# Kernel optimization log

Hardware: AMD Instinct MI355X
Metric: run time of the kernel (lower is better)

Reference implementation:

```python
import jax, jax.numpy as jnp
import numpy as np

B, N, C, L = 32, 1024, 128, 4

def setup_inputs() -> dict:
    key = jax.random.key(0)
    ks = jax.random.split(key, 8)
    x = jax.random.normal(ks[0], (B, N, C), dtype=jnp.float32)
    # binary adjacency: nonzero entries become unit-weight edges (edge weights unused in module)
    adj = jax.random.randint(ks[1], (B, N, N), 0, 2).astype(jnp.float32)
    mask = jnp.ones((B, N), dtype=jnp.float32)
    s = 1.0 / np.sqrt(C)
    weight = jax.random.uniform(ks[2], (L, C, C), minval=-s, maxval=s, dtype=jnp.float32)
    w_ih = jax.random.uniform(ks[3], (L, 3 * C, C), minval=-s, maxval=s, dtype=jnp.float32)
    w_hh = jax.random.uniform(ks[4], (L, 3 * C, C), minval=-s, maxval=s, dtype=jnp.float32)
    b_ih = jax.random.uniform(ks[5], (L, 3 * C), minval=-s, maxval=s, dtype=jnp.float32)
    b_hh = jax.random.uniform(ks[6], (L, 3 * C), minval=-s, maxval=s, dtype=jnp.float32)
    return {"x": x, "adj": adj, "mask": mask, "weight": weight,
            "w_ih": w_ih, "w_hh": w_hh, "b_ih": b_ih, "b_hh": b_hh}

def _gru_cell(m, h, w_ih, w_hh, b_ih, b_hh):
    # PyTorch GRUCell, gate order (r, z, n)
    gx = m @ w_ih.T + b_ih
    gh = h @ w_hh.T + b_hh
    xr, xz, xn = jnp.split(gx, 3, axis=-1)
    hr, hz, hn = jnp.split(gh, 3, axis=-1)
    r = jax.nn.sigmoid(xr + hr)
    z = jax.nn.sigmoid(xz + hz)
    n = jnp.tanh(xn + r * hn)
    return (1.0 - z) * n + z * h

def reference(x, adj, mask, weight, w_ih, w_hh, b_ih, b_hh):
    h = x  # [B, N, C]; in_channels == out_channels so no zero-padding needed
    for i in range(L):
        hw = jnp.einsum('bnc,cd->bnd', h, weight[i])
        # scatter-add of messages source->target == A^T @ (h W), unit edge weights
        m = jnp.einsum('bjn,bjd->bnd', adj, hw)
        h = _gru_cell(m, h, w_ih[i], w_hh[i], b_ih[i], b_hh[i])
    return h * mask[:, :, None]
```

## Files before the change

kernel.cpp:

```cpp
#include <hip/hip_runtime.h>
#include <stdint.h>


#define NB 32
#define NN 1024
#define NC 128
#define NL 4
#define MTOT (NB * NN)

#define KT 64
#define PITCH 72
#define MP 136
#define MSKP 260

typedef __attribute__((ext_vector_type(8))) short s16x8;
typedef __attribute__((ext_vector_type(4))) float f32x4;
typedef __attribute__((ext_vector_type(2))) unsigned int u32x2;
typedef __attribute__((ext_vector_type(4))) unsigned int u32x4;
typedef unsigned short U16;
typedef unsigned int U32;

__device__ __forceinline__ U16 f2bf(float f) {
    union { float f; U32 u; } v; v.f = f;
    return (U16)((v.u + 0x7FFFu + ((v.u >> 16) & 1u)) >> 16);
}
__device__ __forceinline__ float bf2f(U16 h) {
    union { U32 u; float f; } v; v.u = ((U32)h) << 16;
    return v.f;
}
__device__ __forceinline__ void splitbf(float x, U16& hi, U16& lo) {
    hi = f2bf(x);
    lo = f2bf(x - bf2f(hi));
}
__device__ __forceinline__ float sigmoidf_(float x) { return 1.f / (1.f + __expf(-x)); }

__device__ __forceinline__ void glds16(const void* g, void* l) {
    __builtin_amdgcn_global_load_lds(
        (const __attribute__((address_space(1))) void*)g,
        (__attribute__((address_space(3))) void*)l, 16, 0, 0);
}

#define SWZ(row, g) ((row) * 64 + ((((g) ^ ((row) & 7))) * 8))

__global__ __launch_bounds__(256) void k_setup(
    const float* __restrict__ adj, U16* __restrict__ adjT,
    const float* __restrict__ w, const float* __restrict__ wih, const float* __restrict__ whh,
    U16* __restrict__ wThi, U16* __restrict__ wTlo,
    U16* __restrict__ wihhi, U16* __restrict__ wihlo,
    U16* __restrict__ whhhi, U16* __restrict__ whhlo,
    const float* __restrict__ x, U16* __restrict__ hhi, U16* __restrict__ hlo)
{
    __shared__ U32 msk[4 * MSKP];
    const int bid = blockIdx.x, tid = threadIdx.x;
    if (bid < 1024) {
        const int b = bid >> 5, rem = bid & 31;
        const int n0 = (rem >> 3) * 256;
        const int j0 = (rem & 7) * 128;
        const int lane = tid & 63, wv = tid >> 6;
        const int jb = j0 + wv * 32;
        const int nl = n0 + lane * 4;

        U32 mk0 = 0, mk1 = 0, mk2 = 0, mk3 = 0;
#pragma unroll 8
        for (int jj = 0; jj < 32; ++jj) {
            f32x4 v = *(const f32x4*)&adj[((size_t)b << 20) + ((size_t)(jb + jj) << 10) + nl];
            U32 bit = 1u << jj;
            if (v[0] != 0.f) mk0 |= bit;
            if (v[1] != 0.f) mk1 |= bit;
            if (v[2] != 0.f) mk2 |= bit;
            if (v[3] != 0.f) mk3 |= bit;
        }
        u32x4 mv; mv[0] = mk0; mv[1] = mk1; mv[2] = mk2; mv[3] = mk3;
        *(u32x4*)&msk[wv * MSKP + lane * 4] = mv;
        __syncthreads();

#pragma unroll
        for (int p = 0; p < 16; ++p) {
            const int nl2 = p * 16 + (tid >> 4);
            const int c = tid & 15;
            const U32 w32 = msk[(c >> 2) * MSKP + nl2];
            const U32 bits = (w32 >> ((c & 3) * 8)) & 0xffu;
            u32x4 wd;
#pragma unroll
            for (int i = 0; i < 4; ++i) {
                wd[i] = (((bits >> (2 * i)) & 1u) ? 0x00003F80u : 0u)
                      | (((bits >> (2 * i + 1)) & 1u) ? 0x3F800000u : 0u);
            }
            *(u32x4*)&adjT[((size_t)b << 20) + ((size_t)(n0 + nl2) << 10) + j0 + c * 8] = wd;
        }
    } else if (bid < 2816) {
        int i = (bid - 1024) * 256 + tid;
        if (i < 65536) {
            int l = i >> 14, rem = i & 16383, c = rem >> 7, d = rem & 127;
            U16 hi, lo; splitbf(w[i], hi, lo);
            int o = (l << 14) + (d << 7) + c;
            wThi[o] = hi; wTlo[o] = lo;
        } else if (i < 262144) {
            int j = i - 65536;
            U16 hi, lo; splitbf(wih[j], hi, lo);
            wihhi[j] = hi; wihlo[j] = lo;
        } else {
            int j = i - 262144;
            U16 hi, lo; splitbf(whh[j], hi, lo);
            whhhi[j] = hi; whhlo[j] = lo;
        }
    } else {
        const int base = (bid - 2816) * 4096;
#pragma unroll
        for (int g = 0; g < 4; ++g) {
            int i = base + (g * 256 + tid) * 4;
            f32x4 v = *(const f32x4*)&x[i];
            U16 h0, l0, h1, l1, h2, l2, h3, l3;
            splitbf(v[0], h0, l0); splitbf(v[1], h1, l1);
            splitbf(v[2], h2, l2); splitbf(v[3], h3, l3);
            u32x2 ph, pl;
            ph[0] = (U32)h0 | ((U32)h1 << 16); ph[1] = (U32)h2 | ((U32)h3 << 16);
            pl[0] = (U32)l0 | ((U32)l1 << 16); pl[1] = (U32)l2 | ((U32)l3 << 16);
            *(u32x2*)&hhi[i] = ph;
            *(u32x2*)&hlo[i] = pl;
        }
    }
}

struct __align__(16) Smem3 {
    union {
        struct { U16 A[2][128 * PITCH]; U16 B[2][128 * PITCH]; } s;
        float bounce[128 * 129];
    };
};

__global__ __launch_bounds__(256, 2) void k_hw(
    const U16* __restrict__ Ahi, const U16* __restrict__ Alo,
    const U16* __restrict__ Bhi, const U16* __restrict__ Blo,
    U16* __restrict__ Ohi, U16* __restrict__ Olo)
{
    __shared__ Smem3 sm;
    const int tid = threadIdx.x;
    const int lane = tid & 63, wv = tid >> 6;
    const int wr = (wv & 1) * 64, wc = (wv >> 1) * 64;
    const int lm = lane & 15, lk8 = (lane >> 4) * 8;
    const int m0 = blockIdx.x * 128;

    f32x4 acc[4][4] = {};

    for (int kc = 0; kc < 128; kc += KT) {
#pragma unroll
        for (int t = 0; t < 4; ++t) {
            int i = tid + t * 256; int r = i >> 3, v = (i & 7) * 8;
            *(s16x8*)&sm.s.A[0][r * PITCH + v] = *(const s16x8*)&Ahi[(size_t)(m0 + r) * 128 + kc + v];
            *(s16x8*)&sm.s.A[1][r * PITCH + v] = *(const s16x8*)&Alo[(size_t)(m0 + r) * 128 + kc + v];
        }
#pragma unroll
        for (int t = 0; t < 4; ++t) {
            int i = tid + t * 256; int r = i >> 3, v = (i & 7) * 8;
            *(s16x8*)&sm.s.B[0][r * PITCH + v] = *(const s16x8*)&Bhi[r * 128 + kc + v];
            *(s16x8*)&sm.s.B[1][r * PITCH + v] = *(const s16x8*)&Blo[r * 128 + kc + v];
        }
        __syncthreads();
#pragma unroll
        for (int ks = 0; ks < 2; ++ks) {
            const int ko = ks * 32 + lk8;
            s16x8 ahi[4], alo[4], bhi[4], blo[4];
#pragma unroll
            for (int q = 0; q < 4; ++q) {
                ahi[q] = *(const s16x8*)&sm.s.A[0][(wr + q * 16 + lm) * PITCH + ko];
                alo[q] = *(const s16x8*)&sm.s.A[1][(wr + q * 16 + lm) * PITCH + ko];
                bhi[q] = *(const s16x8*)&sm.s.B[0][(wc + q * 16 + lm) * PITCH + ko];
                blo[q] = *(const s16x8*)&sm.s.B[1][(wc + q * 16 + lm) * PITCH + ko];
            }
#pragma unroll
            for (int rt = 0; rt < 4; ++rt)
#pragma unroll
                for (int ct = 0; ct < 4; ++ct) {
                    f32x4 a = acc[rt][ct];
                    a = __builtin_amdgcn_mfma_f32_16x16x32_bf16(ahi[rt], bhi[ct], a, 0, 0, 0);
                    a = __builtin_amdgcn_mfma_f32_16x16x32_bf16(ahi[rt], blo[ct], a, 0, 0, 0);
                    a = __builtin_amdgcn_mfma_f32_16x16x32_bf16(alo[rt], bhi[ct], a, 0, 0, 0);
                    acc[rt][ct] = a;
                }
        }
        __syncthreads();
    }
#pragma unroll
    for (int rt = 0; rt < 4; ++rt)
#pragma unroll
        for (int ct = 0; ct < 4; ++ct)
#pragma unroll
            for (int r = 0; r < 4; ++r)
                sm.bounce[(wr + rt * 16 + (lane >> 4) * 4 + r) * 129 + wc + ct * 16 + lm] = acc[rt][ct][r];
    __syncthreads();
    const int b = m0 >> 10, j0 = m0 & 1023;
    for (int t = 0; t < 32; ++t) {
        int i = tid + t * 256; int d = i >> 6, j2 = (i & 63) * 2;
        float x0 = sm.bounce[j2 * 129 + d], x1 = sm.bounce[(j2 + 1) * 129 + d];
        U16 h0, l0, h1, l1; splitbf(x0, h0, l0); splitbf(x1, h1, l1);
        size_t o = (((size_t)(b * 128 + d)) << 10) + j0 + j2;
        *(U32*)&Ohi[o] = (U32)h0 | ((U32)h1 << 16);
        *(U32*)&Olo[o] = (U32)l0 | ((U32)l1 << 16);
    }
}

__global__ __launch_bounds__(256, 2) void k_mega6(
    const U16* __restrict__ adjT,
    const U16* __restrict__ hwThi, const U16* __restrict__ hwTlo,
    const U16* __restrict__ hhi, const U16* __restrict__ hlo,
    const U16* __restrict__ wihhi, const U16* __restrict__ wihlo,
    const U16* __restrict__ whhhi, const U16* __restrict__ whhlo,
    const float* __restrict__ bih, const float* __restrict__ bhh,
    const float* __restrict__ mask,
    U16* __restrict__ houthi, U16* __restrict__ houtlo,
    float* __restrict__ out, int last)
{
    __shared__ union {
        struct { U16 As[2][64 * 64]; U16 Bh[2][128 * 64]; U16 Bl[2][128 * 64]; } st;
        struct { U16 Mhi[64 * MP]; U16 Mlo[64 * MP]; } m;
    } u;
    const int tid = threadIdx.x;
    const int lane = tid & 63, wv = tid >> 6;
    const int wd0 = wv * 32;
    const int lm = lane & 15, lk8 = (lane >> 4) * 8, quad = lane >> 4;
    const int xcd = blockIdx.x & 7;
    const int j = blockIdx.x >> 3;
    const int bt = xcd * 4 + (j >> 4);
    const int n0 = (j & 15) * 64;
    const int row0 = bt * NN + n0;

#define STAGE(kc, b)                                                                     \
    {                                                                                    \
        _Pragma("unroll")                                                                \
        for (int t = 0; t < 2; ++t) {                                                    \
            int li = tid + t * 256; int r = li >> 3, sg = li & 7;                        \
            glds16(&adjT[((size_t)bt << 20) + ((size_t)(n0 + r) << 10) + (kc)            \
                         + ((sg ^ (r & 7)) * 8)],                                        \
                   &u.st.As[b][li * 8]);                                                 \
        }                                                                                \
        _Pragma("unroll")                                                                \
        for (int t = 0; t < 4; ++t) {                                                    \
            int li = tid + t * 256; int d = li >> 3, sg = li & 7;                        \
            size_t o = (((size_t)(bt * 128 + d)) << 10) + (kc) + ((sg ^ (d & 7)) * 8);   \
            glds16(&hwThi[o], &u.st.Bh[b][li * 8]);                                      \
            glds16(&hwTlo[o], &u.st.Bl[b][li * 8]);                                      \
        }                                                                                \
    }

    f32x4 macc[4][2] = {};
    STAGE(0, 0);
    for (int c = 0; c < 16; ++c) {
        const int b = c & 1;
        __syncthreads();
        if (c + 1 < 16) STAGE((c + 1) * 64, b ^ 1);
#pragma unroll
        for (int ks = 0; ks < 2; ++ks) {
            const int g = ks * 4 + quad;
            s16x8 a[4], bh[2], bl[2];
#pragma unroll
            for (int q = 0; q < 4; ++q)
                a[q] = *(const s16x8*)&u.st.As[b][SWZ(q * 16 + lm, g)];
#pragma unroll
            for (int q = 0; q < 2; ++q) {
                bh[q] = *(const s16x8*)&u.st.Bh[b][SWZ(wd0 + q * 16 + lm, g)];
                bl[q] = *(const s16x8*)&u.st.Bl[b][SWZ(wd0 + q * 16 + lm, g)];
            }
#pragma unroll
            for (int rt = 0; rt < 4; ++rt)
#pragma unroll
                for (int ct = 0; ct < 2; ++ct) {
                    f32x4 cc = macc[rt][ct];
                    cc = __builtin_amdgcn_mfma_f32_16x16x32_bf16(a[rt], bh[ct], cc, 0, 0, 0);
                    cc = __builtin_amdgcn_mfma_f32_16x16x32_bf16(a[rt], bl[ct], cc, 0, 0, 0);
                    macc[rt][ct] = cc;
                }
        }
    }
#undef STAGE
    __syncthreads();

#pragma unroll
    for (int rt = 0; rt < 4; ++rt)
#pragma unroll
        for (int ct = 0; ct < 2; ++ct)
#pragma unroll
            for (int rr = 0; rr < 4; ++rr) {
                int rloc = rt * 16 + quad * 4 + rr;
                int d = wd0 + ct * 16 + lm;
                U16 hi, lo; splitbf(macc[rt][ct][rr], hi, lo);
                u.m.Mhi[rloc * MP + d] = hi;
                u.m.Mlo[rloc * MP + d] = lo;
            }

    f32x4 aR[4][2], aZ[4][2], aXN[4][2], aHN[4][2];
#pragma unroll
    for (int ct = 0; ct < 2; ++ct) {
        const int col = wd0 + ct * 16 + lm;
        const float bR  = bih[col]       + bhh[col];
        const float bZ  = bih[128 + col] + bhh[128 + col];
        const float bXN = bih[256 + col];
        const float bHN = bhh[256 + col];
#pragma unroll
        for (int rt = 0; rt < 4; ++rt) {
            aR[rt][ct]  = f32x4{bR, bR, bR, bR};
            aZ[rt][ct]  = f32x4{bZ, bZ, bZ, bZ};
            aXN[rt][ct] = f32x4{bXN, bXN, bXN, bXN};
            aHN[rt][ct] = f32x4{bHN, bHN, bHN, bHN};
        }
    }

    for (int cc = 0; cc < 4; ++cc) {
        const int ch = (cc + 2) & 3;
        if (cc == 2) __syncthreads();
        const U16* __restrict__ Whi = (ch < 2) ? wihhi : whhhi;
        const U16* __restrict__ Wlo = (ch < 2) ? wihlo : whhlo;
        const int kb = (ch & 1) * 64;
#pragma unroll
        for (int ks = 0; ks < 2; ++ks) {
            const int ko = kb + ks * 32 + lk8;
            s16x8 ahi[4], alo[4];
            if (ch < 2) {
#pragma unroll
                for (int q = 0; q < 4; ++q) {
                    ahi[q] = *(const s16x8*)&u.m.Mhi[(q * 16 + lm) * MP + ko];
                    alo[q] = *(const s16x8*)&u.m.Mlo[(q * 16 + lm) * MP + ko];
                }
            } else {
#pragma unroll
                for (int q = 0; q < 4; ++q) {
                    size_t ao = (size_t)(row0 + q * 16 + lm) * 128 + ko;
                    ahi[q] = *(const s16x8*)&hhi[ao];
                    alo[q] = *(const s16x8*)&hlo[ao];
                }
            }
#pragma unroll
            for (int ct = 0; ct < 2; ++ct) {
                const int col = wd0 + ct * 16 + lm;
                s16x8 bhiR = *(const s16x8*)&Whi[(size_t)col * 128 + ko];
                s16x8 bloR = *(const s16x8*)&Wlo[(size_t)col * 128 + ko];
                s16x8 bhiZ = *(const s16x8*)&Whi[(size_t)(128 + col) * 128 + ko];
                s16x8 bloZ = *(const s16x8*)&Wlo[(size_t)(128 + col) * 128 + ko];
                s16x8 bhiN = *(const s16x8*)&Whi[(size_t)(256 + col) * 128 + ko];
                s16x8 bloN = *(const s16x8*)&Wlo[(size_t)(256 + col) * 128 + ko];
#pragma unroll
                for (int rt = 0; rt < 4; ++rt) {
                    f32x4 r = aR[rt][ct];
                    r = __builtin_amdgcn_mfma_f32_16x16x32_bf16(ahi[rt], bhiR, r, 0, 0, 0);
                    r = __builtin_amdgcn_mfma_f32_16x16x32_bf16(ahi[rt], bloR, r, 0, 0, 0);
                    r = __builtin_amdgcn_mfma_f32_16x16x32_bf16(alo[rt], bhiR, r, 0, 0, 0);
                    aR[rt][ct] = r;
                    f32x4 z = aZ[rt][ct];
                    z = __builtin_amdgcn_mfma_f32_16x16x32_bf16(ahi[rt], bhiZ, z, 0, 0, 0);
                    z = __builtin_amdgcn_mfma_f32_16x16x32_bf16(ahi[rt], bloZ, z, 0, 0, 0);
                    z = __builtin_amdgcn_mfma_f32_16x16x32_bf16(alo[rt], bhiZ, z, 0, 0, 0);
                    aZ[rt][ct] = z;
                }
                if (ch < 2) {
#pragma unroll
                    for (int rt = 0; rt < 4; ++rt) {
                        f32x4 n = aXN[rt][ct];
                        n = __builtin_amdgcn_mfma_f32_16x16x32_bf16(ahi[rt], bhiN, n, 0, 0, 0);
                        n = __builtin_amdgcn_mfma_f32_16x16x32_bf16(ahi[rt], bloN, n, 0, 0, 0);
                        n = __builtin_amdgcn_mfma_f32_16x16x32_bf16(alo[rt], bhiN, n, 0, 0, 0);
                        aXN[rt][ct] = n;
                    }
                } else {
#pragma unroll
                    for (int rt = 0; rt < 4; ++rt) {
                        f32x4 n = aHN[rt][ct];
                        n = __builtin_amdgcn_mfma_f32_16x16x32_bf16(ahi[rt], bhiN, n, 0, 0, 0);
                        n = __builtin_amdgcn_mfma_f32_16x16x32_bf16(ahi[rt], bloN, n, 0, 0, 0);
                        n = __builtin_amdgcn_mfma_f32_16x16x32_bf16(alo[rt], bhiN, n, 0, 0, 0);
                        aHN[rt][ct] = n;
                    }
                }
            }
        }
    }

#pragma unroll
    for (int rt = 0; rt < 4; ++rt) {
#pragma unroll
        for (int ct = 0; ct < 2; ++ct) {
            const int col = wd0 + ct * 16 + lm;
#pragma unroll
            for (int rr = 0; rr < 4; ++rr) {
                const int row = row0 + rt * 16 + quad * 4 + rr;
                float r = sigmoidf_(aR[rt][ct][rr]);
                float z = sigmoidf_(aZ[rt][ct][rr]);
                float n = tanhf(aXN[rt][ct][rr] + r * aHN[rt][ct][rr]);
                size_t ho = (size_t)row * 128 + col;
                float hv = bf2f(hhi[ho]) + bf2f(hlo[ho]);
                float hnew = (1.f - z) * n + z * hv;
                if (last) {
                    out[ho] = hnew * mask[row];
                } else {
                    U16 hi2, lo2; splitbf(hnew, hi2, lo2);
                    houthi[ho] = hi2;
                    houtlo[ho] = lo2;
                }
            }
        }
    }
}

extern "C" void kernel_launch(void* const* d_in, const int* in_sizes, int n_in,
                              void* d_out, int out_size, void* d_ws, size_t ws_size,
                              hipStream_t stream) {
    (void)in_sizes; (void)n_in; (void)out_size; (void)ws_size;
    const float* x    = (const float*)d_in[0];
    const float* adj  = (const float*)d_in[1];
    const float* mask = (const float*)d_in[2];
    const float* wgt  = (const float*)d_in[3];
    const float* wih  = (const float*)d_in[4];
    const float* whh  = (const float*)d_in[5];
    const float* bih  = (const float*)d_in[6];
    const float* bhh  = (const float*)d_in[7];
    float* out = (float*)d_out;

    char* p = (char*)d_ws;
    U16* adjT    = (U16*)p;                p += (size_t)NB * NN * NN * 2;
    U16* h_hi    = (U16*)p;                p += (size_t)MTOT * NC * 2;
    U16* h_lo    = (U16*)p;                p += (size_t)MTOT * NC * 2;
    U16* hwT_hi  = (U16*)p;                p += (size_t)NB * NC * NN * 2;
    U16* hwT_lo  = (U16*)p;                p += (size_t)NB * NC * NN * 2;
    U16* wT_hi   = (U16*)p;                p += (size_t)NL * NC * NC * 2;
    U16* wT_lo   = (U16*)p;                p += (size_t)NL * NC * NC * 2;
    U16* wih_hi  = (U16*)p;                p += (size_t)NL * 384 * NC * 2;
    U16* wih_lo  = (U16*)p;                p += (size_t)NL * 384 * NC * 2;
    U16* whh_hi  = (U16*)p;                p += (size_t)NL * 384 * NC * 2;
    U16* whh_lo  = (U16*)p;                p += (size_t)NL * 384 * NC * 2;

    k_setup<<<3840, 256, 0, stream>>>(adj, adjT, wgt, wih, whh,
                                      wT_hi, wT_lo, wih_hi, wih_lo, whh_hi, whh_lo,
                                      x, h_hi, h_lo);

    for (int l = 0; l < NL; ++l) {
        k_hw<<<256, 256, 0, stream>>>(h_hi, h_lo,
                                      wT_hi + l * 16384, wT_lo + l * 16384,
                                      hwT_hi, hwT_lo);
        k_mega6<<<512, 256, 0, stream>>>(adjT, hwT_hi, hwT_lo, h_hi, h_lo,
                                         wih_hi + l * 49152, wih_lo + l * 49152,
                                         whh_hi + l * 49152, whh_lo + l * 49152,
                                         bih + l * 384, bhh + l * 384, mask,
                                         h_hi, h_lo, out, (l == NL - 1) ? 1 : 0);
    }
}
```

Baseline: 507.7 us.

## Store adjacency as packed bitmask and expand to bf16 in LDS on the fly

The setup kernel now writes the transposed adjacency as packed bits (64 U16 words per row) instead of a full bf16 matrix. The aggregation kernel reads these bit words and expands them into swizzled bf16 ones and zeros directly in shared memory, replacing the async global-to-LDS loads of the dense adjacency tile. This cuts adjacency traffic per layer by 16x and shrinks the setup write, but adds ALU work and regular LDS stores inside the pipelined K loop.

```diff
diff --git a/kernel.cpp b/kernel.cpp
--- a/kernel.cpp
+++ b/kernel.cpp
@@ -43,7 +43,7 @@
 #define SWZ(row, g) ((row) * 64 + ((((g) ^ ((row) & 7))) * 8))
 
 __global__ __launch_bounds__(256) void k_setup(
-    const float* __restrict__ adj, U16* __restrict__ adjT,
+    const float* __restrict__ adj, U16* __restrict__ adjB,
     const float* __restrict__ w, const float* __restrict__ wih, const float* __restrict__ whh,
     U16* __restrict__ wThi, U16* __restrict__ wTlo,
     U16* __restrict__ wihhi, U16* __restrict__ wihlo,
@@ -74,20 +74,12 @@
         *(u32x4*)&msk[wv * MSKP + lane * 4] = mv;
         __syncthreads();
 
-#pragma unroll
-        for (int p = 0; p < 16; ++p) {
-            const int nl2 = p * 16 + (tid >> 4);
-            const int c = tid & 15;
-            const U32 w32 = msk[(c >> 2) * MSKP + nl2];
-            const U32 bits = (w32 >> ((c & 3) * 8)) & 0xffu;
-            u32x4 wd;
-#pragma unroll
-            for (int i = 0; i < 4; ++i) {
-                wd[i] = (((bits >> (2 * i)) & 1u) ? 0x00003F80u : 0u)
-                      | (((bits >> (2 * i + 1)) & 1u) ? 0x3F800000u : 0u);
-            }
-            *(u32x4*)&adjT[((size_t)b << 20) + ((size_t)(n0 + nl2) << 10) + j0 + c * 8] = wd;
-        }
+        u32x4 wd;
+        wd[0] = msk[0 * MSKP + tid];
+        wd[1] = msk[1 * MSKP + tid];
+        wd[2] = msk[2 * MSKP + tid];
+        wd[3] = msk[3 * MSKP + tid];
+        *(u32x4*)&adjB[(((size_t)b << 10) + n0 + tid) * 64 + (rem & 7) * 8] = wd;
     } else if (bid < 2816) {
         int i = (bid - 1024) * 256 + tid;
         if (i < 65536) {
@@ -200,8 +192,8 @@
     }
 }
 
-__global__ __launch_bounds__(256, 2) void k_mega6(
-    const U16* __restrict__ adjT,
+__global__ __launch_bounds__(256, 2) void k_mega7(
+    const U16* __restrict__ adjB,
     const U16* __restrict__ hwThi, const U16* __restrict__ hwTlo,
     const U16* __restrict__ hhi, const U16* __restrict__ hlo,
     const U16* __restrict__ wihhi, const U16* __restrict__ wihlo,
@@ -211,7 +203,7 @@
     U16* __restrict__ houthi, U16* __restrict__ houtlo,
     float* __restrict__ out, int last)
 {
-    __shared__ union {
+    __shared__ __align__(16) union {
         struct { U16 As[2][64 * 64]; U16 Bh[2][128 * 64]; U16 Bl[2][128 * 64]; } st;
         struct { U16 Mhi[64 * MP]; U16 Mlo[64 * MP]; } m;
     } u;
@@ -225,30 +217,55 @@
     const int n0 = (j & 15) * 64;
     const int row0 = bt * NN + n0;
 
-#define STAGE(kc, b)                                                                     \
-    {                                                                                    \
-        _Pragma("unroll")                                                                \
-        for (int t = 0; t < 2; ++t) {                                                    \
-            int li = tid + t * 256; int r = li >> 3, sg = li & 7;                        \
-            glds16(&adjT[((size_t)bt << 20) + ((size_t)(n0 + r) << 10) + (kc)            \
-                         + ((sg ^ (r & 7)) * 8)],                                        \
-                   &u.st.As[b][li * 8]);                                                 \
-        }                                                                                \
-        _Pragma("unroll")                                                                \
-        for (int t = 0; t < 4; ++t) {                                                    \
-            int li = tid + t * 256; int d = li >> 3, sg = li & 7;                        \
-            size_t o = (((size_t)(bt * 128 + d)) << 10) + (kc) + ((sg ^ (d & 7)) * 8);   \
-            glds16(&hwThi[o], &u.st.Bh[b][li * 8]);                                      \
-            glds16(&hwTlo[o], &u.st.Bl[b][li * 8]);                                      \
-        }                                                                                \
+    const int er  = tid >> 2;
+    const int ea  = tid & 3;
+    const int ex  = er & 7;
+    const int ea2 = ea ^ (er & 3);
+    const int eB0h = (2 * (ea2 ^ (ex >> 1))) >> 1;
+    const int es1 = 2 * ea2 + (er & 1);
+    const int es2 = 2 * ea2 + 1 - (er & 1);
+    const int esh1 = 8 * ((es1 ^ ex) & 1);
+    const int esh2 = 8 * ((es2 ^ ex) & 1);
+    const U16* __restrict__ mrow = adjB + (((size_t)bt << 10) + n0 + er) * 64;
+
+#define EXPA(c, b)                                                                        \
+    {                                                                                     \
+        U32 v = mrow[(c) * 4 + eB0h];                                                     \
+        U32 by1 = (v >> esh1) & 0xffu;                                                    \
+        U32 by2 = (v >> esh2) & 0xffu;                                                    \
+        u32x4 w1, w2;                                                                     \
+        _Pragma("unroll")                                                                 \
+        for (int i = 0; i < 4; ++i) {                                                     \
+            w1[i] = (((by1 >> (2 * i)) & 1u) ? 0x00003F80u : 0u)                          \
+                  | (((by1 >> (2 * i + 1)) & 1u) ? 0x3F800000u : 0u);                     \
+            w2[i] = (((by2 >> (2 * i)) & 1u) ? 0x00003F80u : 0u)                          \
+                  | (((by2 >> (2 * i + 1)) & 1u) ? 0x3F800000u : 0u);                     \
+        }                                                                                 \
+        *(u32x4*)&u.st.As[b][er * 64 + es1 * 8] = w1;                                     \
+        *(u32x4*)&u.st.As[b][er * 64 + es2 * 8] = w2;                                     \
+    }
+
+#define STAGE_B(kc, b)                                                                    \
+    {                                                                                     \
+        _Pragma("unroll")                                                                 \
+        for (int t = 0; t < 4; ++t) {                                                     \
+            int li = tid + t * 256; int d = li >> 3, sg = li & 7;                         \
+            size_t o = (((size_t)(bt * 128 + d)) << 10) + (kc) + ((sg ^ (d & 7)) * 8);    \
+            glds16(&hwThi[o], &u.st.Bh[b][li * 8]);                                       \
+            glds16(&hwTlo[o], &u.st.Bl[b][li * 8]);                                       \
+        }                                                                                 \
     }
 
     f32x4 macc[4][2] = {};
-    STAGE(0, 0);
+    STAGE_B(0, 0);
+    EXPA(0, 0);
     for (int c = 0; c < 16; ++c) {
         const int b = c & 1;
         __syncthreads();
-        if (c + 1 < 16) STAGE((c + 1) * 64, b ^ 1);
+        if (c + 1 < 16) {
+            STAGE_B((c + 1) * 64, b ^ 1);
+            EXPA(c + 1, b ^ 1);
+        }
 #pragma unroll
         for (int ks = 0; ks < 2; ++ks) {
             const int g = ks * 4 + quad;
@@ -272,7 +289,8 @@
                 }
         }
     }
-#undef STAGE
+#undef STAGE_B
+#undef EXPA
     __syncthreads();
 
 #pragma unroll
@@ -415,7 +433,7 @@
     float* out = (float*)d_out;
 
     char* p = (char*)d_ws;
-    U16* adjT    = (U16*)p;                p += (size_t)NB * NN * NN * 2;
+    U16* adjB    = (U16*)p;                p += (size_t)NB * NN * 64 * 2;
     U16* h_hi    = (U16*)p;                p += (size_t)MTOT * NC * 2;
     U16* h_lo    = (U16*)p;                p += (size_t)MTOT * NC * 2;
     U16* hwT_hi  = (U16*)p;                p += (size_t)NB * NC * NN * 2;
@@ -427,7 +445,7 @@
     U16* whh_hi  = (U16*)p;                p += (size_t)NL * 384 * NC * 2;
     U16* whh_lo  = (U16*)p;                p += (size_t)NL * 384 * NC * 2;
 
-    k_setup<<<3840, 256, 0, stream>>>(adj, adjT, wgt, wih, whh,
+    k_setup<<<3840, 256, 0, stream>>>(adj, adjB, wgt, wih, whh,
                                       wT_hi, wT_lo, wih_hi, wih_lo, whh_hi, whh_lo,
                                       x, h_hi, h_lo);
 
@@ -435,7 +453,7 @@
         k_hw<<<256, 256, 0, stream>>>(h_hi, h_lo,
                                       wT_hi + l * 16384, wT_lo + l * 16384,
                                       hwT_hi, hwT_lo);
-        k_mega6<<<512, 256, 0, stream>>>(adjT, hwT_hi, hwT_lo, h_hi, h_lo,
+        k_mega7<<<512, 256, 0, stream>>>(adjB, hwT_hi, hwT_lo, h_hi, h_lo,
                                          wih_hi + l * 49152, wih_lo + l * 49152,
                                          whh_hi + l * 49152, whh_lo + l * 49152,
                                          bih + l * 384, bhh + l * 384, mask,
```

Measured after the change: 521.4 us. +2.7%, slower.

## Halve aggregation K-tile and split GRU column tiles to raise occupancy

Applied to the files above, without the earlier changes.

The adjacency-aggregation loop now stages 32-wide K tiles instead of 64, using a new 4-group swizzle. This halves shared-memory staging and doubles the iteration count. The GRU gate stage processes its two column tiles one after another, so fewer accumulators are live, and launch bounds are raised to three blocks per CU. The aim is lower LDS and register pressure for more resident waves. The cost is more barriers per K and reloading the h and weight operands once per column tile.

```diff
diff --git a/kernel.cpp b/kernel.cpp
--- a/kernel.cpp
+++ b/kernel.cpp
@@ -8,7 +8,6 @@
 #define NL 4
 #define MTOT (NB * NN)
 
-#define KT 64
 #define PITCH 72
 #define MP 136
 #define MSKP 260
@@ -40,7 +39,7 @@
         (__attribute__((address_space(3))) void*)l, 16, 0, 0);
 }
 
-#define SWZ(row, g) ((row) * 64 + ((((g) ^ ((row) & 7))) * 8))
+#define SWZ32(row, g) ((row) * 32 + ((((g) ^ (((row) >> 1) & 3))) * 8))
 
 __global__ __launch_bounds__(256) void k_setup(
     const float* __restrict__ adj, U16* __restrict__ adjT,
@@ -143,7 +142,7 @@
 
     f32x4 acc[4][4] = {};
 
-    for (int kc = 0; kc < 128; kc += KT) {
+    for (int kc = 0; kc < 128; kc += 64) {
 #pragma unroll
         for (int t = 0; t < 4; ++t) {
             int i = tid + t * 256; int r = i >> 3, v = (i & 7) * 8;
@@ -200,7 +199,7 @@
     }
 }
 
-__global__ __launch_bounds__(256, 2) void k_mega6(
+__global__ __launch_bounds__(256, 3) void k_mega9(
     const U16* __restrict__ adjT,
     const U16* __restrict__ hwThi, const U16* __restrict__ hwTlo,
     const U16* __restrict__ hhi, const U16* __restrict__ hlo,
@@ -211,8 +210,8 @@
     U16* __restrict__ houthi, U16* __restrict__ houtlo,
     float* __restrict__ out, int last)
 {
-    __shared__ union {
-        struct { U16 As[2][64 * 64]; U16 Bh[2][128 * 64]; U16 Bl[2][128 * 64]; } st;
+    __shared__ __align__(16) union {
+        struct { U16 As[2][64 * 32]; U16 Bh[2][128 * 32]; U16 Bl[2][128 * 32]; } st;
         struct { U16 Mhi[64 * MP]; U16 Mlo[64 * MP]; } m;
     } u;
     const int tid = threadIdx.x;
@@ -225,52 +224,47 @@
     const int n0 = (j & 15) * 64;
     const int row0 = bt * NN + n0;
 
-#define STAGE(kc, b)                                                                     \
-    {                                                                                    \
-        _Pragma("unroll")                                                                \
-        for (int t = 0; t < 2; ++t) {                                                    \
-            int li = tid + t * 256; int r = li >> 3, sg = li & 7;                        \
-            glds16(&adjT[((size_t)bt << 20) + ((size_t)(n0 + r) << 10) + (kc)            \
-                         + ((sg ^ (r & 7)) * 8)],                                        \
-                   &u.st.As[b][li * 8]);                                                 \
-        }                                                                                \
-        _Pragma("unroll")                                                                \
-        for (int t = 0; t < 4; ++t) {                                                    \
-            int li = tid + t * 256; int d = li >> 3, sg = li & 7;                        \
-            size_t o = (((size_t)(bt * 128 + d)) << 10) + (kc) + ((sg ^ (d & 7)) * 8);   \
-            glds16(&hwThi[o], &u.st.Bh[b][li * 8]);                                      \
-            glds16(&hwTlo[o], &u.st.Bl[b][li * 8]);                                      \
-        }                                                                                \
+    const int srA = tid >> 2, ssA = tid & 3;
+    const int skA = ((ssA ^ ((srA >> 1) & 3)) * 8);
+
+#define STAGE(kc, b)                                                                   \
+    {                                                                                  \
+        glds16(&adjT[((size_t)bt << 20) + ((size_t)(n0 + srA) << 10) + (kc) + skA],    \
+               &u.st.As[b][tid * 8]);                                                  \
+        _Pragma("unroll")                                                              \
+        for (int t = 0; t < 2; ++t) {                                                  \
+            int li = tid + t * 256; int d = li >> 2, sg = li & 3;                      \
+            size_t o = (((size_t)(bt * 128 + d)) << 10) + (kc)                         \
+                       + ((sg ^ ((d >> 1) & 3)) * 8);                                  \
+            glds16(&hwThi[o], &u.st.Bh[b][li * 8]);                                    \
+            glds16(&hwTlo[o], &u.st.Bl[b][li * 8]);                                    \
+        }                                                                              \
     }
 
     f32x4 macc[4][2] = {};
     STAGE(0, 0);
-    for (int c = 0; c < 16; ++c) {
+    for (int c = 0; c < 32; ++c) {
         const int b = c & 1;
         __syncthreads();
-        if (c + 1 < 16) STAGE((c + 1) * 64, b ^ 1);
-#pragma unroll
-        for (int ks = 0; ks < 2; ++ks) {
-            const int g = ks * 4 + quad;
-            s16x8 a[4], bh[2], bl[2];
-#pragma unroll
-            for (int q = 0; q < 4; ++q)
-                a[q] = *(const s16x8*)&u.st.As[b][SWZ(q * 16 + lm, g)];
-#pragma unroll
-            for (int q = 0; q < 2; ++q) {
-                bh[q] = *(const s16x8*)&u.st.Bh[b][SWZ(wd0 + q * 16 + lm, g)];
-                bl[q] = *(const s16x8*)&u.st.Bl[b][SWZ(wd0 + q * 16 + lm, g)];
-            }
-#pragma unroll
-            for (int rt = 0; rt < 4; ++rt)
-#pragma unroll
-                for (int ct = 0; ct < 2; ++ct) {
-                    f32x4 cc = macc[rt][ct];
-                    cc = __builtin_amdgcn_mfma_f32_16x16x32_bf16(a[rt], bh[ct], cc, 0, 0, 0);
-                    cc = __builtin_amdgcn_mfma_f32_16x16x32_bf16(a[rt], bl[ct], cc, 0, 0, 0);
-                    macc[rt][ct] = cc;
-                }
-        }
+        if (c + 1 < 32) STAGE((c + 1) * 32, b ^ 1);
+        s16x8 a[4], bh[2], bl[2];
+#pragma unroll
+        for (int q = 0; q < 4; ++q)
+            a[q] = *(const s16x8*)&u.st.As[b][SWZ32(q * 16 + lm, quad)];
+#pragma unroll
+        for (int q = 0; q < 2; ++q) {
+            bh[q] = *(const s16x8*)&u.st.Bh[b][SWZ32(wd0 + q * 16 + lm, quad)];
+            bl[q] = *(const s16x8*)&u.st.Bl[b][SWZ32(wd0 + q * 16 + lm, quad)];
+        }
+#pragma unroll
+        for (int rt = 0; rt < 4; ++rt)
+#pragma unroll
+            for (int ct = 0; ct < 2; ++ct) {
+                f32x4 cc = macc[rt][ct];
+                cc = __builtin_amdgcn_mfma_f32_16x16x32_bf16(a[rt], bh[ct], cc, 0, 0, 0);
+                cc = __builtin_amdgcn_mfma_f32_16x16x32_bf16(a[rt], bl[ct], cc, 0, 0, 0);
+                macc[rt][ct] = cc;
+            }
     }
 #undef STAGE
     __syncthreads();
@@ -288,50 +282,45 @@
                 u.m.Mlo[rloc * MP + d] = lo;
             }
 
-    f32x4 aR[4][2], aZ[4][2], aXN[4][2], aHN[4][2];
-#pragma unroll
-    for (int ct = 0; ct < 2; ++ct) {
-        const int col = wd0 + ct * 16 + lm;
+    for (int ctp = 0; ctp < 2; ++ctp) {
+        const int col = wd0 + ctp * 16 + lm;
         const float bR  = bih[col]       + bhh[col];
         const float bZ  = bih[128 + col] + bhh[128 + col];
         const float bXN = bih[256 + col];
         const float bHN = bhh[256 + col];
+        f32x4 aR[4], aZ[4], aXN[4], aHN[4];
 #pragma unroll
         for (int rt = 0; rt < 4; ++rt) {
-            aR[rt][ct]  = f32x4{bR, bR, bR, bR};
-            aZ[rt][ct]  = f32x4{bZ, bZ, bZ, bZ};
-            aXN[rt][ct] = f32x4{bXN, bXN, bXN, bXN};
-            aHN[rt][ct] = f32x4{bHN, bHN, bHN, bHN};
-        }
-    }
-
-    for (int cc = 0; cc < 4; ++cc) {
-        const int ch = (cc + 2) & 3;
-        if (cc == 2) __syncthreads();
-        const U16* __restrict__ Whi = (ch < 2) ? wihhi : whhhi;
-        const U16* __restrict__ Wlo = (ch < 2) ? wihlo : whhlo;
-        const int kb = (ch & 1) * 64;
-#pragma unroll
-        for (int ks = 0; ks < 2; ++ks) {
-            const int ko = kb + ks * 32 + lk8;
-            s16x8 ahi[4], alo[4];
-            if (ch < 2) {
-#pragma unroll
-                for (int q = 0; q < 4; ++q) {
-                    ahi[q] = *(const s16x8*)&u.m.Mhi[(q * 16 + lm) * MP + ko];
-                    alo[q] = *(const s16x8*)&u.m.Mlo[(q * 16 + lm) * MP + ko];
+            aR[rt]  = f32x4{bR, bR, bR, bR};
+            aZ[rt]  = f32x4{bZ, bZ, bZ, bZ};
+            aXN[rt] = f32x4{bXN, bXN, bXN, bXN};
+            aHN[rt] = f32x4{bHN, bHN, bHN, bHN};
+        }
+
+        for (int cc = 0; cc < 4; ++cc) {
+            const int ch = (cc + 2) & 3;
+            if (ctp == 0 && cc == 2) __syncthreads();
+            const U16* __restrict__ Whi = (ch < 2) ? wihhi : whhhi;
+            const U16* __restrict__ Wlo = (ch < 2) ? wihlo : whhlo;
+            const int kb = (ch & 1) * 64;
+#pragma unroll
+            for (int ks = 0; ks < 2; ++ks) {
+                const int ko = kb + ks * 32 + lk8;
+                s16x8 ahi[4], alo[4];
+                if (ch < 2) {
+#pragma unroll
+                    for (int q = 0; q < 4; ++q) {
+                        ahi[q] = *(const s16x8*)&u.m.Mhi[(q * 16 + lm) * MP + ko];
+                        alo[q] = *(const s16x8*)&u.m.Mlo[(q * 16 + lm) * MP + ko];
+                    }
+                } else {
+#pragma unroll
+                    for (int q = 0; q < 4; ++q) {
+                        size_t ao = (size_t)(row0 + q * 16 + lm) * 128 + ko;
+                        ahi[q] = *(const s16x8*)&hhi[ao];
+                        alo[q] = *(const s16x8*)&hlo[ao];
+                    }
                 }
-            } else {
-#pragma unroll
-                for (int q = 0; q < 4; ++q) {
-                    size_t ao = (size_t)(row0 + q * 16 + lm) * 128 + ko;
-                    ahi[q] = *(const s16x8*)&hhi[ao];
-                    alo[q] = *(const s16x8*)&hlo[ao];
-                }
-            }
-#pragma unroll
-            for (int ct = 0; ct < 2; ++ct) {
-                const int col = wd0 + ct * 16 + lm;
                 s16x8 bhiR = *(const s16x8*)&Whi[(size_t)col * 128 + ko];
                 s16x8 bloR = *(const s16x8*)&Wlo[(size_t)col * 128 + ko];
                 s16x8 bhiZ = *(const s16x8*)&Whi[(size_t)(128 + col) * 128 + ko];
@@ -340,51 +329,47 @@
                 s16x8 bloN = *(const s16x8*)&Wlo[(size_t)(256 + col) * 128 + ko];
 #pragma unroll
                 for (int rt = 0; rt < 4; ++rt) {
-                    f32x4 r = aR[rt][ct];
+                    f32x4 r = aR[rt];
                     r = __builtin_amdgcn_mfma_f32_16x16x32_bf16(ahi[rt], bhiR, r, 0, 0, 0);
                     r = __builtin_amdgcn_mfma_f32_16x16x32_bf16(ahi[rt], bloR, r, 0, 0, 0);
                     r = __builtin_amdgcn_mfma_f32_16x16x32_bf16(alo[rt], bhiR, r, 0, 0, 0);
-                    aR[rt][ct] = r;
-                    f32x4 z = aZ[rt][ct];
+                    aR[rt] = r;
+                    f32x4 z = aZ[rt];
                     z = __builtin_amdgcn_mfma_f32_16x16x32_bf16(ahi[rt], bhiZ, z, 0, 0, 0);
                     z = __builtin_amdgcn_mfma_f32_16x16x32_bf16(ahi[rt], bloZ, z, 0, 0, 0);
                     z = __builtin_amdgcn_mfma_f32_16x16x32_bf16(alo[rt], bhiZ, z, 0, 0, 0);
-                    aZ[rt][ct] = z;
+                    aZ[rt] = z;
                 }
                 if (ch < 2) {
 #pragma unroll
                     for (int rt = 0; rt < 4; ++rt) {
-                        f32x4 n = aXN[rt][ct];
+                        f32x4 n = aXN[rt];
                         n = __builtin_amdgcn_mfma_f32_16x16x32_bf16(ahi[rt], bhiN, n, 0, 0, 0);
                         n = __builtin_amdgcn_mfma_f32_16x16x32_bf16(ahi[rt], bloN, n, 0, 0, 0);
                         n = __builtin_amdgcn_mfma_f32_16x16x32_bf16(alo[rt], bhiN, n, 0, 0, 0);
-                        aXN[rt][ct] = n;
+                        aXN[rt] = n;
                     }
                 } else {
 #pragma unroll
                     for (int rt = 0; rt < 4; ++rt) {
-                        f32x4 n = aHN[rt][ct];
+                        f32x4 n = aHN[rt];
                         n = __builtin_amdgcn_mfma_f32_16x16x32_bf16(ahi[rt], bhiN, n, 0, 0, 0);
                         n = __builtin_amdgcn_mfma_f32_16x16x32_bf16(ahi[rt], bloN, n, 0, 0, 0);
                         n = __builtin_amdgcn_mfma_f32_16x16x32_bf16(alo[rt], bhiN, n, 0, 0, 0);
-                        aHN[rt][ct] = n;
+                        aHN[rt] = n;
                     }
                 }
             }
         }
-    }
-
-#pragma unroll
-    for (int rt = 0; rt < 4; ++rt) {
-#pragma unroll
-        for (int ct = 0; ct < 2; ++ct) {
-            const int col = wd0 + ct * 16 + lm;
+
+#pragma unroll
+        for (int rt = 0; rt < 4; ++rt) {
 #pragma unroll
             for (int rr = 0; rr < 4; ++rr) {
                 const int row = row0 + rt * 16 + quad * 4 + rr;
-                float r = sigmoidf_(aR[rt][ct][rr]);
-                float z = sigmoidf_(aZ[rt][ct][rr]);
-                float n = tanhf(aXN[rt][ct][rr] + r * aHN[rt][ct][rr]);
+                float r = sigmoidf_(aR[rt][rr]);
+                float z = sigmoidf_(aZ[rt][rr]);
+                float n = tanhf(aXN[rt][rr] + r * aHN[rt][rr]);
                 size_t ho = (size_t)row * 128 + col;
                 float hv = bf2f(hhi[ho]) + bf2f(hlo[ho]);
                 float hnew = (1.f - z) * n + z * hv;
@@ -435,7 +420,7 @@
         k_hw<<<256, 256, 0, stream>>>(h_hi, h_lo,
                                       wT_hi + l * 16384, wT_lo + l * 16384,
                                       hwT_hi, hwT_lo);
-        k_mega6<<<512, 256, 0, stream>>>(adjT, hwT_hi, hwT_lo, h_hi, h_lo,
+        k_mega9<<<512, 256, 0, stream>>>(adjT, hwT_hi, hwT_lo, h_hi, h_lo,
                                          wih_hi + l * 49152, wih_lo + l * 49152,
                                          whh_hi + l * 49152, whh_lo + l * 49152,
                                          bih + l * 384, bhh + l * 384, mask,
```

Result: slower. 722.6 us (+42.3%).

## Load adjacency GEMM operands directly from global into registers, dropping LDS staging

Applied to the files above, without the earlier changes.

The aggregation GEMM in the fused GRU kernel no longer stages adjacency and hw tiles through double-buffered LDS via global_load_lds. Each lane now loads its MFMA fragments straight from global memory into registers, with a two-deep register ping-pong, and the in-loop __syncthreads are gone. The aim is to cut LDS traffic and barrier stalls. In exchange, rows are no longer shared across waves, so the four waves each re-read the same adjacency rows from global/L2, and the per-lane 16-byte loads are strided. This may expose memory latency.

```diff
diff --git a/kernel.cpp b/kernel.cpp
--- a/kernel.cpp
+++ b/kernel.cpp
@@ -8,7 +8,6 @@
 #define NL 4
 #define MTOT (NB * NN)
 
-#define KT 64
 #define PITCH 72
 #define MP 136
 #define MSKP 260
@@ -33,14 +32,6 @@
     lo = f2bf(x - bf2f(hi));
 }
 __device__ __forceinline__ float sigmoidf_(float x) { return 1.f / (1.f + __expf(-x)); }
-
-__device__ __forceinline__ void glds16(const void* g, void* l) {
-    __builtin_amdgcn_global_load_lds(
-        (const __attribute__((address_space(1))) void*)g,
-        (__attribute__((address_space(3))) void*)l, 16, 0, 0);
-}
-
-#define SWZ(row, g) ((row) * 64 + ((((g) ^ ((row) & 7))) * 8))
 
 __global__ __launch_bounds__(256) void k_setup(
     const float* __restrict__ adj, U16* __restrict__ adjT,
@@ -143,7 +134,7 @@
 
     f32x4 acc[4][4] = {};
 
-    for (int kc = 0; kc < 128; kc += KT) {
+    for (int kc = 0; kc < 128; kc += 64) {
 #pragma unroll
         for (int t = 0; t < 4; ++t) {
             int i = tid + t * 256; int r = i >> 3, v = (i & 7) * 8;
@@ -200,7 +191,7 @@
     }
 }
 
-__global__ __launch_bounds__(256, 2) void k_mega6(
+__global__ __launch_bounds__(256, 2) void k_mega10(
     const U16* __restrict__ adjT,
     const U16* __restrict__ hwThi, const U16* __restrict__ hwTlo,
     const U16* __restrict__ hhi, const U16* __restrict__ hlo,
@@ -211,10 +202,7 @@
     U16* __restrict__ houthi, U16* __restrict__ houtlo,
     float* __restrict__ out, int last)
 {
-    __shared__ union {
-        struct { U16 As[2][64 * 64]; U16 Bh[2][128 * 64]; U16 Bl[2][128 * 64]; } st;
-        struct { U16 Mhi[64 * MP]; U16 Mlo[64 * MP]; } m;
-    } u;
+    __shared__ __align__(16) struct { U16 Mhi[64 * MP]; U16 Mlo[64 * MP]; } m;
     const int tid = threadIdx.x;
     const int lane = tid & 63, wv = tid >> 6;
     const int wd0 = wv * 32;
@@ -225,55 +213,47 @@
     const int n0 = (j & 15) * 64;
     const int row0 = bt * NN + n0;
 
-#define STAGE(kc, b)                                                                     \
-    {                                                                                    \
-        _Pragma("unroll")                                                                \
-        for (int t = 0; t < 2; ++t) {                                                    \
-            int li = tid + t * 256; int r = li >> 3, sg = li & 7;                        \
-            glds16(&adjT[((size_t)bt << 20) + ((size_t)(n0 + r) << 10) + (kc)            \
-                         + ((sg ^ (r & 7)) * 8)],                                        \
-                   &u.st.As[b][li * 8]);                                                 \
-        }                                                                                \
-        _Pragma("unroll")                                                                \
-        for (int t = 0; t < 4; ++t) {                                                    \
-            int li = tid + t * 256; int d = li >> 3, sg = li & 7;                        \
-            size_t o = (((size_t)(bt * 128 + d)) << 10) + (kc) + ((sg ^ (d & 7)) * 8);   \
-            glds16(&hwThi[o], &u.st.Bh[b][li * 8]);                                      \
-            glds16(&hwTlo[o], &u.st.Bl[b][li * 8]);                                      \
-        }                                                                                \
+    const size_t abase = ((size_t)bt << 20) + ((size_t)n0 << 10) + ((size_t)lm << 10);
+    const size_t bbase = (((size_t)(bt * 128 + wd0 + lm)) << 10);
+
+#define LOADF(kk, A, BH, BL)                                                              \
+    {                                                                                     \
+        const int ko = (kk) * 32 + quad * 8;                                              \
+        _Pragma("unroll")                                                                 \
+        for (int q = 0; q < 4; ++q)                                                       \
+            A[q] = *(const s16x8*)&adjT[abase + ((size_t)q << 14) + ko];                  \
+        _Pragma("unroll")                                                                 \
+        for (int q = 0; q < 2; ++q) {                                                     \
+            size_t o = bbase + ((size_t)q << 14) + ko;                                    \
+            BH[q] = *(const s16x8*)&hwThi[o];                                             \
+            BL[q] = *(const s16x8*)&hwTlo[o];                                             \
+        }                                                                                 \
+    }
+
+#define MM(A, BH, BL)                                                                     \
+    {                                                                                     \
+        _Pragma("unroll")                                                                 \
+        for (int rt = 0; rt < 4; ++rt)                                                    \
+            _Pragma("unroll")                                                             \
+            for (int ct = 0; ct < 2; ++ct) {                                              \
+                f32x4 cc = macc[rt][ct];                                                  \
+                cc = __builtin_amdgcn_mfma_f32_16x16x32_bf16(A[rt], BH[ct], cc, 0, 0, 0); \
+                cc = __builtin_amdgcn_mfma_f32_16x16x32_bf16(A[rt], BL[ct], cc, 0, 0, 0); \
+                macc[rt][ct] = cc;                                                        \
+            }                                                                             \
     }
 
     f32x4 macc[4][2] = {};
-    STAGE(0, 0);
-    for (int c = 0; c < 16; ++c) {
-        const int b = c & 1;
-        __syncthreads();
-        if (c + 1 < 16) STAGE((c + 1) * 64, b ^ 1);
-#pragma unroll
-        for (int ks = 0; ks < 2; ++ks) {
-            const int g = ks * 4 + quad;
-            s16x8 a[4], bh[2], bl[2];
-#pragma unroll
-            for (int q = 0; q < 4; ++q)
-                a[q] = *(const s16x8*)&u.st.As[b][SWZ(q * 16 + lm, g)];
-#pragma unroll
-            for (int q = 0; q < 2; ++q) {
-                bh[q] = *(const s16x8*)&u.st.Bh[b][SWZ(wd0 + q * 16 + lm, g)];
-                bl[q] = *(const s16x8*)&u.st.Bl[b][SWZ(wd0 + q * 16 + lm, g)];
-            }
-#pragma unroll
-            for (int rt = 0; rt < 4; ++rt)
-#pragma unroll
-                for (int ct = 0; ct < 2; ++ct) {
-                    f32x4 cc = macc[rt][ct];
-                    cc = __builtin_amdgcn_mfma_f32_16x16x32_bf16(a[rt], bh[ct], cc, 0, 0, 0);
-                    cc = __builtin_amdgcn_mfma_f32_16x16x32_bf16(a[rt], bl[ct], cc, 0, 0, 0);
-                    macc[rt][ct] = cc;
-                }
-        }
-    }
-#undef STAGE
-    __syncthreads();
+    s16x8 aA[4], bhA[2], blA[2], aB[4], bhB[2], blB[2];
+    LOADF(0, aA, bhA, blA);
+    for (int kk = 0; kk < 32; kk += 2) {
+        LOADF(kk + 1, aB, bhB, blB);
+        MM(aA, bhA, blA);
+        if (kk + 2 < 32) LOADF(kk + 2, aA, bhA, blA);
+        MM(aB, bhB, blB);
+    }
+#undef LOADF
+#undef MM
 
 #pragma unroll
     for (int rt = 0; rt < 4; ++rt)
@@ -284,8 +264,8 @@
                 int rloc = rt * 16 + quad * 4 + rr;
                 int d = wd0 + ct * 16 + lm;
                 U16 hi, lo; splitbf(macc[rt][ct][rr], hi, lo);
-                u.m.Mhi[rloc * MP + d] = hi;
-                u.m.Mlo[rloc * MP + d] = lo;
+                m.Mhi[rloc * MP + d] = hi;
+                m.Mlo[rloc * MP + d] = lo;
             }
 
     f32x4 aR[4][2], aZ[4][2], aXN[4][2], aHN[4][2];
@@ -318,8 +298,8 @@
             if (ch < 2) {
 #pragma unroll
                 for (int q = 0; q < 4; ++q) {
-                    ahi[q] = *(const s16x8*)&u.m.Mhi[(q * 16 + lm) * MP + ko];
-                    alo[q] = *(const s16x8*)&u.m.Mlo[(q * 16 + lm) * MP + ko];
+                    ahi[q] = *(const s16x8*)&m.Mhi[(q * 16 + lm) * MP + ko];
+                    alo[q] = *(const s16x8*)&m.Mlo[(q * 16 + lm) * MP + ko];
                 }
             } else {
 #pragma unroll
@@ -435,10 +415,10 @@
         k_hw<<<256, 256, 0, stream>>>(h_hi, h_lo,
                                       wT_hi + l * 16384, wT_lo + l * 16384,
                                       hwT_hi, hwT_lo);
-        k_mega6<<<512, 256, 0, stream>>>(adjT, hwT_hi, hwT_lo, h_hi, h_lo,
-                                         wih_hi + l * 49152, wih_lo + l * 49152,
-                                         whh_hi + l * 49152, whh_lo + l * 49152,
-                                         bih + l * 384, bhh + l * 384, mask,
-                                         h_hi, h_lo, out, (l == NL - 1) ? 1 : 0);
-    }
-}
+        k_mega10<<<512, 256, 0, stream>>>(adjT, hwT_hi, hwT_lo, h_hi, h_lo,
+                                          wih_hi + l * 49152, wih_lo + l * 49152,
+                                          whh_hi + l * 49152, whh_lo + l * 49152,
+                                          bih + l * 384, bhh + l * 384, mask,
+                                          h_hi, h_lo, out, (l == NL - 1) ? 1 : 0);
+    }
+}
```

New measurement: 673.9 us. 32.7% more time.
